# Performance work log

Hardware: AMD Instinct MI355X
Metric: run time of the kernel (lower is better)

The kernel has to match this reference:

```python
import jax, jax.numpy as jnp
import numpy as np

B, T, D, H = 4, 2048, 1024, 16
DK = D // H  # 64


def setup_inputs() -> dict:
    key = jax.random.key(0)
    ks = jax.random.split(key, 7)
    s = 1.0 / np.sqrt(D)
    x = jax.random.normal(ks[0], (B, T, D), dtype=jnp.float32)
    W_qkv = jax.random.normal(ks[1], (D, 3 * D), dtype=jnp.float32) * s
    b_qkv = jnp.zeros((3 * D,), dtype=jnp.float32)
    W_out = jax.random.normal(ks[2], (D, D), dtype=jnp.float32) * s
    b_out = jnp.zeros((D,), dtype=jnp.float32)
    # rotary tables: standard inv-freq construction, shape [T, DK//2]
    inv_freq = 1.0 / (10000.0 ** (np.arange(0, DK, 2, dtype=np.float32) / DK))
    ang = jnp.asarray(np.arange(T, dtype=np.float32)[:, None] * inv_freq[None, :])
    cos = jnp.cos(ang)
    sin = jnp.sin(ang)
    return {"x": x, "W_qkv": W_qkv, "b_qkv": b_qkv, "W_out": W_out,
            "b_out": b_out, "cos": cos, "sin": sin}


def _rope(t, cos, sin):
    # t: [B, H, T, DK]; cos/sin: [T, DK//2] broadcast over B, H
    t1, t2 = t[..., ::2], t[..., 1::2]
    return jnp.concatenate([t1 * cos - t2 * sin, t1 * sin + t2 * cos], axis=-1)


def reference(x, W_qkv, b_qkv, W_out, b_out, cos, sin):
    Bx, Tx, C = x.shape
    dk = C // H
    qkv = (x @ W_qkv + b_qkv).reshape(Bx, Tx, H, 3 * dk).transpose(0, 2, 1, 3)
    q, k, v = jnp.split(qkv, 3, axis=-1)  # each [B, H, T, dk]
    q = _rope(q, cos, sin)
    k = _rope(k, cos, sin)
    scores = jnp.einsum("bhtd,bhsd->bhts", q, k) / jnp.sqrt(jnp.float32(dk))
    causal = jnp.tril(jnp.ones((Tx, Tx), dtype=bool))  # [T, T]
    scores = jnp.where(causal, scores, jnp.float32(-jnp.inf))
    w = jax.nn.softmax(scores, axis=-1)  # dropout p=0.0 (eval): identity
    attn = jnp.einsum("bhts,bhsd->bhtd", w, v)
    attn = attn.transpose(0, 2, 1, 3).reshape(Bx, Tx, C)
    return attn @ W_out + b_out
```

## Files before the change

kernel.cpp:

```cpp
#include <hip/hip_runtime.h>
#include <cmath>

typedef __attribute__((ext_vector_type(4))) float f32x4;
typedef __attribute__((ext_vector_type(16))) float f32x16;
typedef __attribute__((ext_vector_type(8))) __bf16 bf16x8;
typedef __attribute__((ext_vector_type(8))) short s16x8;
typedef __attribute__((ext_vector_type(2))) unsigned int u32x2;

#define CB 4
#define CT 2048
#define CD 1024
#define CH 16
#define CDK 64
#define CBT 8192
#define CBH 64

#define GLOAD_LDS16(g, l)                                              \
  __builtin_amdgcn_global_load_lds(                                    \
      (const __attribute__((address_space(1))) unsigned int*)(g),      \
      (__attribute__((address_space(3))) unsigned int*)(l), 16, 0, 0)

__device__ __forceinline__ unsigned short f2bf(float f) {
  union { float f; unsigned u; } x; x.f = f;
  unsigned r = x.u + 0x7fffu + ((x.u >> 16) & 1u);
  return (unsigned short)(r >> 16);
}
__device__ __forceinline__ float bf2f(unsigned short b) {
  union { unsigned u; float f; } x; x.u = ((unsigned)b) << 16;
  return x.f;
}
__device__ __forceinline__ f32x4 mfma16(bf16x8 a, bf16x8 b, f32x4 c) {
  return __builtin_amdgcn_mfma_f32_16x16x32_bf16(a, b, c, 0, 0, 0);
}
__device__ __forceinline__ f32x16 mfma32(bf16x8 a, bf16x8 b, f32x16 c) {
  return __builtin_amdgcn_mfma_f32_32x32x16_bf16(a, b, c, 0, 0, 0);
}
__device__ __forceinline__ unsigned cvtpk(float lo, float hi) {
  unsigned r;
  asm("v_cvt_pk_bf16_f32 %0, %1, %2" : "=v"(r) : "v"(lo), "v"(hi));
  return r;
}

__global__ void convert_f32_bf16(const float* __restrict__ src,
                                 unsigned short* __restrict__ dst, int n) {
  int i = (blockIdx.x * blockDim.x + threadIdx.x) * 4;
  if (i >= n) return;
  float4 v = *(const float4*)(src + i);
  ushort4 o;
  o.x = f2bf(v.x); o.y = f2bf(v.y); o.z = f2bf(v.z); o.w = f2bf(v.w);
  *(ushort4*)(dst + i) = o;
}

__global__ void transpose_weights(const float* __restrict__ wqkv,
                                  unsigned short* __restrict__ wqt,
                                  const float* __restrict__ wout,
                                  unsigned short* __restrict__ wot) {
  __shared__ float tile[32][33];
  const int x = threadIdx.x, y0 = threadIdx.y;
  const int bx = blockIdx.x, rt = blockIdx.y;
  const float* src;
  unsigned short* dst;
  int C, ct;
  if (bx < 96) { src = wqkv; dst = wqt; C = 3072; ct = bx; }
  else         { src = wout; dst = wot; C = 1024; ct = bx - 96; }
  const int R = 1024;
#pragma unroll
  for (int k = 0; k < 4; ++k) {
    int r = rt * 32 + y0 + k * 8;
    tile[y0 + k * 8][x] = src[(size_t)r * C + ct * 32 + x];
  }
  __syncthreads();
#pragma unroll
  for (int k = 0; k < 4; ++k) {
    int c = ct * 32 + y0 + k * 8;
    dst[(size_t)c * R + rt * 32 + x] = f2bf(tile[x][y0 + k * 8]);
  }
}

template <int MODE>
__global__ __launch_bounds__(256, 4) void gemm_bt(
    const unsigned short* __restrict__ A, const unsigned short* __restrict__ Bt,
    const float* __restrict__ bias, unsigned short* __restrict__ o0,
    unsigned short* __restrict__ o1, unsigned short* __restrict__ o2,
    float* __restrict__ fout, const float* __restrict__ cosT,
    const float* __restrict__ sinT, int M, int N, int K) {
  __shared__ __align__(16) unsigned short As[128 * 64];
  __shared__ __align__(16) unsigned short Bs[128 * 64];
  const int tid = threadIdx.x;
  const int lane = tid & 63, wid = tid >> 6;
  const int wr = wid >> 1, wc = wid & 1;
  const int m0 = blockIdx.x * 128, n0 = blockIdx.y * 128;
  const int l15 = lane & 15, l4 = lane >> 4;
  const int rx = l15 & 7;

  f32x4 acc[4][4];
#pragma unroll
  for (int i = 0; i < 4; ++i)
#pragma unroll
    for (int j = 0; j < 4; ++j) acc[i][j] = (f32x4){0.f, 0.f, 0.f, 0.f};

  const int srow = tid >> 3;
  const int scol = ((tid & 7) ^ (srow & 7)) * 8;
  const unsigned short* ag = A + (size_t)(m0 + srow) * K + scol;
  const unsigned short* bg = Bt + (size_t)(n0 + srow) * K + scol;
  unsigned short* asd = As + wid * 512;
  unsigned short* bsd = Bs + wid * 512;

  for (int k0 = 0; k0 < K; k0 += 64) {
#pragma unroll
    for (int p = 0; p < 4; ++p) {
      GLOAD_LDS16(ag + (size_t)(p * 32) * K + k0, asd + p * 2048);
      GLOAD_LDS16(bg + (size_t)(p * 32) * K + k0, bsd + p * 2048);
    }
    __syncthreads();
#pragma unroll
    for (int kk = 0; kk < 2; ++kk) {
      const int gsw = ((kk * 4 + l4) ^ rx) * 8;
      bf16x8 af[4], bfr[4];
#pragma unroll
      for (int i = 0; i < 4; ++i)
        af[i] = *(const bf16x8*)(&As[(wr * 64 + i * 16 + l15) * 64 + gsw]);
#pragma unroll
      for (int j = 0; j < 4; ++j)
        bfr[j] = *(const bf16x8*)(&Bs[(wc * 64 + j * 16 + l15) * 64 + gsw]);
#pragma unroll
      for (int i = 0; i < 4; ++i)
#pragma unroll
        for (int j = 0; j < 4; ++j)
          acc[i][j] = mfma16(af[i], bfr[j], acc[i][j]);
    }
    __syncthreads();
  }

  if (MODE == 1) {
#pragma unroll
    for (int i = 0; i < 4; ++i)
#pragma unroll
      for (int j = 0; j < 4; ++j) {
        const int row0 = m0 + wr * 64 + i * 16 + l4 * 4;
        const int col = n0 + wc * 64 + j * 16 + l15;
        const float bv = bias[col];
#pragma unroll
        for (int r = 0; r < 4; ++r)
          fout[(size_t)(row0 + r) * N + col] = acc[i][j][r] + bv;
      }
  } else {
#pragma unroll
    for (int i = 0; i < 4; ++i)
#pragma unroll
      for (int j = 0; j < 4; ++j) {
        const int col = n0 + wc * 64 + j * 16 + l15;
        const float bv = bias[col];
        const int h = col / 192;
        const int c = col % 192;
        const int sel = c >> 6;
        const int d = c & 63;
        if (sel < 2) {
          const int p = d >> 1;
          const bool even = (d & 1) == 0;
          const float qsc = (sel == 0) ? 0.18033688011112042592f : 1.0f;
          unsigned short* dst = (sel == 0) ? o0 : o1;
          const int dout = even ? p : (p + 32);
#pragma unroll
          for (int r = 0; r < 4; ++r) {
            const int row = m0 + wr * 64 + i * 16 + l4 * 4 + r;
            const int b = row >> 11, t = row & 2047;
            const float v = acc[i][j][r] + bv;
            const float vp = __shfl_xor(v, 1);
            const float cs = cosT[t * 32 + p];
            const float sn = sinT[t * 32 + p];
            const float ve = even ? v : vp;
            const float vo = even ? vp : v;
            const float res = (even ? (ve * cs - vo * sn)
                                    : (ve * sn + vo * cs)) * qsc;
            dst[((size_t)((b * CH + h) * CT + t)) * CDK + dout] = f2bf(res);
          }
        } else {
#pragma unroll
          for (int r = 0; r < 4; ++r) {
            const int row = m0 + wr * 64 + i * 16 + l4 * 4 + r;
            const int b = row >> 11, t = row & 2047;
            o2[((size_t)((b * CH + h) * CDK + d)) * CT + t] =
                f2bf(acc[i][j][r] + bv);
          }
        }
      }
  }
}

__global__ __launch_bounds__(512, 4) void attn_fwd5(
    const unsigned short* __restrict__ qg, const unsigned short* __restrict__ kg,
    const unsigned short* __restrict__ vtg, unsigned short* __restrict__ ctx) {
  __shared__ __align__(16) unsigned short smem[24576];
  unsigned short* Ks = smem;
  unsigned short* Vt = smem + 12288;
  const int tid = threadIdx.x, lane = tid & 63, w = tid >> 6;
  const int l31 = lane & 31, hi = lane >> 5;
  const int b1 = blockIdx.x;
  const int g8 = b1 & 7, idx8 = b1 >> 3;
  const int qb = 7 - (idx8 & 7);
  const int bh = g8 + 8 * (idx8 >> 3);
  const unsigned short* qp = qg + ((size_t)bh * CT + qb * 256) * CDK;
  const unsigned short* kp = kg + (size_t)bh * CT * CDK;
  const unsigned short* vp = vtg + (size_t)bh * CDK * CT;

  bf16x8 qf[4];
  {
    const unsigned short* qrow = qp + (size_t)(w * 32 + l31) * CDK + hi * 8;
#pragma unroll
    for (int ks = 0; ks < 4; ++ks) qf[ks] = *(const bf16x8*)(qrow + ks * 16);
  }
#pragma unroll
  for (int ks = 0; ks < 4; ++ks)
    asm volatile("" :: "v"(*(const f32x4*)&qf[ks]));

  const int lr = lane >> 3;
  const int srow = w * 8 + lr;
  const int gsw = ((lane & 7) ^ lr) * 8;
  const unsigned short* ksrc = kp + (size_t)srow * CDK + gsw;
  const unsigned short* vsrc = vp + (size_t)srow * CT + gsw;
  const int ldo = w * 512;

  const int NJ = 4 * qb + 4;
  const int njw = ((qb * 256 + w * 32 + 31) >> 6) + 1;
  const int qrow_g = qb * 256 + w * 32 + l31;

  auto STAGE = [&](int t, int buf) {
    GLOAD_LDS16(ksrc + (size_t)t * 64 * CDK, Ks + buf * 4096 + ldo);
    GLOAD_LDS16(vsrc + (size_t)t * 64, Vt + buf * 4096 + ldo);
  };

  f32x16 oacc[2];
#pragma unroll
  for (int nb = 0; nb < 2; ++nb)
#pragma unroll
    for (int r = 0; r < 16; ++r) oacc[nb][r] = 0.f;
  float lsum = 0.f;

  STAGE(0, 0);
  STAGE(1, 1);

  int b0 = 0;
  for (int j = 0; j < NJ; ++j) {
    int bp = b0 + 2; if (bp > 2) bp -= 3;
    if (j + 2 < NJ) STAGE(j + 2, bp);
    const int pend = NJ - 1 - j;
    if (pend >= 2)      asm volatile("s_waitcnt vmcnt(4)" ::: "memory");
    else if (pend == 1) asm volatile("s_waitcnt vmcnt(2)" ::: "memory");
    else                asm volatile("s_waitcnt vmcnt(0)" ::: "memory");
    __builtin_amdgcn_s_barrier();

    if (j < njw) {
      const unsigned short* KB = Ks + b0 * 4096;
      const unsigned short* VB = Vt + b0 * 4096;

      f32x16 pacc[2];
      __builtin_amdgcn_s_setprio(1);
#pragma unroll
      for (int kb = 0; kb < 2; ++kb) {
#pragma unroll
        for (int r = 0; r < 16; ++r) pacc[kb][r] = 0.f;
#pragma unroll
        for (int ks = 0; ks < 4; ++ks) {
          const int row = kb * 32 + l31;
          bf16x8 kf = *(const bf16x8*)(KB + row * 64 + (((ks * 2 + hi) ^ (row & 7)) * 8));
          pacc[kb] = mfma32(kf, qf[ks], pacc[kb]);
        }
      }
      __builtin_amdgcn_s_setprio(0);

      if (j == njw - 1) {
        const int key0 = j * 64;
#pragma unroll
        for (int kb = 0; kb < 2; ++kb)
#pragma unroll
          for (int r = 0; r < 16; ++r) {
            const int key = key0 + kb * 32 + (r & 3) + 8 * (r >> 2) + 4 * hi;
            if (key > qrow_g) pacc[kb][r] = -1e30f;
          }
      }

#pragma unroll
      for (int kb = 0; kb < 2; ++kb)
#pragma unroll
        for (int r = 0; r < 16; ++r)
          pacc[kb][r] = __builtin_amdgcn_exp2f(pacc[kb][r]);
      float rs;
      {
        float t[16];
#pragma unroll
        for (int r = 0; r < 16; ++r) t[r] = pacc[0][r] + pacc[1][r];
#pragma unroll
        for (int s = 8; s > 0; s >>= 1)
#pragma unroll
          for (int r = 0; r < s; ++r) t[r] += t[r + s];
        rs = t[0];
      }
      {
        unsigned ru = __float_as_uint(rs);
        u32x2 sw = __builtin_amdgcn_permlane32_swap(ru, ru, false, false);
        rs += __uint_as_float(hi ? sw[0] : sw[1]);
      }
      lsum += rs;

      bf16x8 pf[4];
#pragma unroll
      for (int kb = 0; kb < 2; ++kb)
#pragma unroll
        for (int half = 0; half < 2; ++half) {
          const int b0i = half * 8;
          unsigned c0 = cvtpk(pacc[kb][b0i + 0], pacc[kb][b0i + 1]);
          unsigned c1 = cvtpk(pacc[kb][b0i + 2], pacc[kb][b0i + 3]);
          unsigned c2 = cvtpk(pacc[kb][b0i + 4], pacc[kb][b0i + 5]);
          unsigned c3 = cvtpk(pacc[kb][b0i + 6], pacc[kb][b0i + 7]);
          u32x2 r02 = __builtin_amdgcn_permlane32_swap(c0, c2, false, false);
          u32x2 r13 = __builtin_amdgcn_permlane32_swap(c1, c3, false, false);
          union { unsigned u[4]; bf16x8 v; } fr;
          fr.u[0] = r02[0]; fr.u[1] = r13[0]; fr.u[2] = r02[1]; fr.u[3] = r13[1];
          pf[kb * 2 + half] = fr.v;
        }

      __builtin_amdgcn_s_setprio(1);
#pragma unroll
      for (int nb = 0; nb < 2; ++nb)
#pragma unroll
        for (int ks = 0; ks < 4; ++ks) {
          const int row = nb * 32 + l31;
          bf16x8 vf = *(const bf16x8*)(VB + row * 64 + (((ks * 2 + hi) ^ (row & 7)) * 8));
          oacc[nb] = mfma32(vf, pf[ks], oacc[nb]);
        }
      __builtin_amdgcn_s_setprio(0);
    }

    __builtin_amdgcn_s_barrier();
    b0 = (b0 == 2) ? 0 : b0 + 1;
  }

  __syncthreads();

  unsigned short* tr = smem + w * 2048;
  const float inv = 1.f / lsum;
#pragma unroll
  for (int nb = 0; nb < 2; ++nb)
#pragma unroll
    for (int rp = 0; rp < 8; ++rp) {
      const int r = rp * 2;
      unsigned pkd = cvtpk(oacc[nb][r] * inv, oacc[nb][r + 1] * inv);
      const int d = nb * 32 + (r & 3) + 8 * (r >> 2) + 4 * hi;
      const int g = (d >> 3) ^ (l31 & 7);
      *(unsigned*)(tr + l31 * 64 + g * 8 + (d & 7)) = pkd;
    }
  const int b = bh >> 4, h = bh & 15;
#pragma unroll
  for (int s = 0; s < 4; ++s) {
    const int c = s * 64 + lane;
    const int qr = c >> 3, g = c & 7;
    s16x8 row = *(const s16x8*)(tr + qr * 64 + ((g ^ (qr & 7))) * 8);
    const int tok = qb * 256 + w * 32 + qr;
    *(s16x8*)(ctx + ((size_t)(b * CT + tok)) * CD + h * CDK + g * 8) = row;
  }
}

extern "C" void kernel_launch(void* const* d_in, const int* in_sizes, int n_in,
                              void* d_out, int out_size, void* d_ws, size_t ws_size,
                              hipStream_t stream) {
  (void)in_sizes; (void)n_in; (void)out_size; (void)ws_size;
  const float* x     = (const float*)d_in[0];
  const float* W_qkv = (const float*)d_in[1];
  const float* b_qkv = (const float*)d_in[2];
  const float* W_out = (const float*)d_in[3];
  const float* b_out = (const float*)d_in[4];
  const float* cosT  = (const float*)d_in[5];
  const float* sinT  = (const float*)d_in[6];
  float* out = (float*)d_out;

  unsigned short* xb   = (unsigned short*)d_ws;
  unsigned short* wqt  = xb + (size_t)CBT * CD;
  unsigned short* wot  = wqt + (size_t)3 * CD * CD;
  unsigned short* qbuf = wot + (size_t)CD * CD;
  unsigned short* kbuf = qbuf + (size_t)CBH * CT * CDK;
  unsigned short* vbuf = kbuf + (size_t)CBH * CT * CDK;
  unsigned short* ctx  = vbuf + (size_t)CBH * CT * CDK;

  {
    int n = CBT * CD;
    convert_f32_bf16<<<n / (256 * 4), 256, 0, stream>>>(x, xb, n);
  }
  transpose_weights<<<dim3(128, 32), dim3(32, 8), 0, stream>>>(
      W_qkv, wqt, W_out, wot);
  gemm_bt<0><<<dim3(CBT / 128, 3 * CD / 128), 256, 0, stream>>>(
      xb, wqt, b_qkv, qbuf, kbuf, vbuf, nullptr, cosT, sinT, CBT, 3 * CD, CD);
  attn_fwd5<<<dim3(512), 512, 0, stream>>>(qbuf, kbuf, vbuf, ctx);
  gemm_bt<1><<<dim3(CBT / 128, CD / 128), 256, 0, stream>>>(
      ctx, wot, b_out, nullptr, nullptr, nullptr, out, nullptr, nullptr,
      CBT, CD, CD);
}
```

Baseline: 166.5 us.

## Quad-buffer attention K/V to drop barrier, merge prep kernels, vectorize stores

The attention kernel moves from three to four LDS buffers for K/V tiles, indexed by j&3. With a prefetch distance of two, the buffer being filled never overlaps one still being read, so the trailing per-iteration barrier is removed. The input conversion and weight transpose are merged into one launch. In the QKV GEMM epilogue, RoPE writes rotated q/k in interleaved order (a consistent permutation of the head dimension that leaves q·k unchanged) using sign arithmetic instead of selects, and V^T stores become packed 4-element writes. The extra LDS buffer raises shared memory per block, which may reduce occupancy.

After: 161.4 us. 1.03x faster.

```diff
diff --git a/kernel.cpp b/kernel.cpp
--- a/kernel.cpp
+++ b/kernel.cpp
@@ -41,23 +41,25 @@
   return r;
 }
 
-__global__ void convert_f32_bf16(const float* __restrict__ src,
-                                 unsigned short* __restrict__ dst, int n) {
-  int i = (blockIdx.x * blockDim.x + threadIdx.x) * 4;
-  if (i >= n) return;
-  float4 v = *(const float4*)(src + i);
-  ushort4 o;
-  o.x = f2bf(v.x); o.y = f2bf(v.y); o.z = f2bf(v.z); o.w = f2bf(v.w);
-  *(ushort4*)(dst + i) = o;
-}
-
-__global__ void transpose_weights(const float* __restrict__ wqkv,
-                                  unsigned short* __restrict__ wqt,
-                                  const float* __restrict__ wout,
-                                  unsigned short* __restrict__ wot) {
+__global__ void prep_inputs(const float* __restrict__ x,
+                            unsigned short* __restrict__ xb,
+                            const float* __restrict__ wqkv,
+                            unsigned short* __restrict__ wqt,
+                            const float* __restrict__ wout,
+                            unsigned short* __restrict__ wot) {
   __shared__ float tile[32][33];
-  const int x = threadIdx.x, y0 = threadIdx.y;
-  const int bx = blockIdx.x, rt = blockIdx.y;
+  const int b = blockIdx.x, tid = threadIdx.x;
+  if (b < 8192) {
+    const int i = (b * 256 + tid) * 4;
+    float4 v = *(const float4*)(x + i);
+    ushort4 o;
+    o.x = f2bf(v.x); o.y = f2bf(v.y); o.z = f2bf(v.z); o.w = f2bf(v.w);
+    *(ushort4*)(xb + i) = o;
+    return;
+  }
+  const int bt = b - 8192;
+  const int bx = bt & 127, rt = bt >> 7;
+  const int xx = tid & 31, y0 = tid >> 5;
   const float* src;
   unsigned short* dst;
   int C, ct;
@@ -67,13 +69,13 @@
 #pragma unroll
   for (int k = 0; k < 4; ++k) {
     int r = rt * 32 + y0 + k * 8;
-    tile[y0 + k * 8][x] = src[(size_t)r * C + ct * 32 + x];
+    tile[y0 + k * 8][xx] = src[(size_t)r * C + ct * 32 + xx];
   }
   __syncthreads();
 #pragma unroll
   for (int k = 0; k < 4; ++k) {
     int c = ct * 32 + y0 + k * 8;
-    dst[(size_t)c * R + rt * 32 + x] = f2bf(tile[x][y0 + k * 8]);
+    dst[(size_t)c * R + rt * 32 + xx] = f2bf(tile[xx][y0 + k * 8]);
   }
 }
 
@@ -157,10 +159,9 @@
         const int d = c & 63;
         if (sel < 2) {
           const int p = d >> 1;
-          const bool even = (d & 1) == 0;
+          const float sgn = (d & 1) ? 1.0f : -1.0f;
           const float qsc = (sel == 0) ? 0.18033688011112042592f : 1.0f;
           unsigned short* dst = (sel == 0) ? o0 : o1;
-          const int dout = even ? p : (p + 32);
 #pragma unroll
           for (int r = 0; r < 4; ++r) {
             const int row = m0 + wr * 64 + i * 16 + l4 * 4 + r;
@@ -169,31 +170,29 @@
             const float vp = __shfl_xor(v, 1);
             const float cs = cosT[t * 32 + p];
             const float sn = sinT[t * 32 + p];
-            const float ve = even ? v : vp;
-            const float vo = even ? vp : v;
-            const float res = (even ? (ve * cs - vo * sn)
-                                    : (ve * sn + vo * cs)) * qsc;
-            dst[((size_t)((b * CH + h) * CT + t)) * CDK + dout] = f2bf(res);
+            const float res = (v * cs + sgn * vp * sn) * qsc;
+            dst[((size_t)((b * CH + h) * CT + t)) * CDK + d] = f2bf(res);
           }
         } else {
-#pragma unroll
-          for (int r = 0; r < 4; ++r) {
-            const int row = m0 + wr * 64 + i * 16 + l4 * 4 + r;
-            const int b = row >> 11, t = row & 2047;
-            o2[((size_t)((b * CH + h) * CDK + d)) * CT + t] =
-                f2bf(acc[i][j][r] + bv);
-          }
+          const int t0g = m0 + wr * 64 + i * 16 + l4 * 4;
+          const int b = t0g >> 11, t = t0g & 2047;
+          ushort4 pk;
+          pk.x = f2bf(acc[i][j][0] + bv);
+          pk.y = f2bf(acc[i][j][1] + bv);
+          pk.z = f2bf(acc[i][j][2] + bv);
+          pk.w = f2bf(acc[i][j][3] + bv);
+          *(ushort4*)(&o2[((size_t)((b * CH + h) * CDK + d)) * CT + t]) = pk;
         }
       }
   }
 }
 
-__global__ __launch_bounds__(512, 4) void attn_fwd5(
+__global__ __launch_bounds__(512, 4) void attn_fwd6(
     const unsigned short* __restrict__ qg, const unsigned short* __restrict__ kg,
     const unsigned short* __restrict__ vtg, unsigned short* __restrict__ ctx) {
-  __shared__ __align__(16) unsigned short smem[24576];
+  __shared__ __align__(16) unsigned short smem[32768];
   unsigned short* Ks = smem;
-  unsigned short* Vt = smem + 12288;
+  unsigned short* Vt = smem + 16384;
   const int tid = threadIdx.x, lane = tid & 63, w = tid >> 6;
   const int l31 = lane & 31, hi = lane >> 5;
   const int b1 = blockIdx.x;
@@ -225,7 +224,8 @@
   const int njw = ((qb * 256 + w * 32 + 31) >> 6) + 1;
   const int qrow_g = qb * 256 + w * 32 + l31;
 
-  auto STAGE = [&](int t, int buf) {
+  auto STAGE = [&](int t) {
+    const int buf = t & 3;
     GLOAD_LDS16(ksrc + (size_t)t * 64 * CDK, Ks + buf * 4096 + ldo);
     GLOAD_LDS16(vsrc + (size_t)t * 64, Vt + buf * 4096 + ldo);
   };
@@ -237,13 +237,11 @@
     for (int r = 0; r < 16; ++r) oacc[nb][r] = 0.f;
   float lsum = 0.f;
 
-  STAGE(0, 0);
-  STAGE(1, 1);
-
-  int b0 = 0;
+  STAGE(0);
+  STAGE(1);
+
   for (int j = 0; j < NJ; ++j) {
-    int bp = b0 + 2; if (bp > 2) bp -= 3;
-    if (j + 2 < NJ) STAGE(j + 2, bp);
+    if (j + 2 < NJ) STAGE(j + 2);
     const int pend = NJ - 1 - j;
     if (pend >= 2)      asm volatile("s_waitcnt vmcnt(4)" ::: "memory");
     else if (pend == 1) asm volatile("s_waitcnt vmcnt(2)" ::: "memory");
@@ -251,8 +249,8 @@
     __builtin_amdgcn_s_barrier();
 
     if (j < njw) {
-      const unsigned short* KB = Ks + b0 * 4096;
-      const unsigned short* VB = Vt + b0 * 4096;
+      const unsigned short* KB = Ks + (j & 3) * 4096;
+      const unsigned short* VB = Vt + (j & 3) * 4096;
 
       f32x16 pacc[2];
       __builtin_amdgcn_s_setprio(1);
@@ -331,9 +329,6 @@
         }
       __builtin_amdgcn_s_setprio(0);
     }
-
-    __builtin_amdgcn_s_barrier();
-    b0 = (b0 == 2) ? 0 : b0 + 1;
   }
 
   __syncthreads();
@@ -382,15 +377,11 @@
   unsigned short* vbuf = kbuf + (size_t)CBH * CT * CDK;
   unsigned short* ctx  = vbuf + (size_t)CBH * CT * CDK;
 
-  {
-    int n = CBT * CD;
-    convert_f32_bf16<<<n / (256 * 4), 256, 0, stream>>>(x, xb, n);
-  }
-  transpose_weights<<<dim3(128, 32), dim3(32, 8), 0, stream>>>(
-      W_qkv, wqt, W_out, wot);
+  prep_inputs<<<dim3(8192 + 4096), 256, 0, stream>>>(x, xb, W_qkv, wqt,
+                                                     W_out, wot);
   gemm_bt<0><<<dim3(CBT / 128, 3 * CD / 128), 256, 0, stream>>>(
       xb, wqt, b_qkv, qbuf, kbuf, vbuf, nullptr, cosT, sinT, CBT, 3 * CD, CD);
-  attn_fwd5<<<dim3(512), 512, 0, stream>>>(qbuf, kbuf, vbuf, ctx);
+  attn_fwd6<<<dim3(512), 512, 0, stream>>>(qbuf, kbuf, vbuf, ctx);
   gemm_bt<1><<<dim3(CBT / 128, CD / 128), 256, 0, stream>>>(
       ctx, wot, b_out, nullptr, nullptr, nullptr, out, nullptr, nullptr,
       CBT, CD, CD);
```
